# Performance work log

Measured on AMD Instinct MI355X. Metric: run time of the kernel, lower is better.

## Reference

```python
import jax, jax.numpy as jnp
import numpy as np

WIN = 5            # LNCC window_size
W_IMG = 1.0        # image_loss_weight
W_SMOOTH = 0.02    # smoothness_weight
W_JAC = 0.01       # jacobian_weight
W_INV = 0.1        # inverse_consistency_weight
EPS = 1e-05


def _avg_pool3d(x, k):
    # matches F.avg_pool3d(kernel=k, stride=1, padding=k//2, count_include_pad=True)
    p = k // 2
    s = jax.lax.reduce_window(x, jnp.array(0.0, x.dtype), jax.lax.add,
                              (1, 1, k, k, k), (1, 1, 1, 1, 1),
                              [(0, 0), (0, 0), (p, p), (p, p), (p, p)])
    return s / (k ** 3)


def _lncc(source, target):
    conv = lambda v: _avg_pool3d(v, WIN)
    sm, tm = conv(source), conv(target)
    sv = conv(source * source) - sm * sm
    tv = conv(target * target) - tm * tm
    cross = conv(source * target) - sm * tm
    lncc = cross * cross / (sv * tv + EPS)
    return jnp.nan_to_num(1.0 - lncc.mean(), nan=1.0, posinf=1.0, neginf=1.0)


def _grad3d_l2(disp):
    # Grad3D(penalty='l2'): mean squared forward differences per axis
    dz = disp[:, :, 1:] - disp[:, :, :-1]
    dy = disp[:, :, :, 1:] - disp[:, :, :, :-1]
    dx = disp[:, :, :, :, 1:] - disp[:, :, :, :, :-1]
    return (jnp.mean(dz * dz) + jnp.mean(dy * dy) + jnp.mean(dx * dx)) / 3.0


def _neg_jacobian(d):
    dx = d[:, :, 1:, :-1, :-1] - d[:, :, :-1, :-1, :-1]
    dy = d[:, :, :-1, 1:, :-1] - d[:, :, :-1, :-1, :-1]
    dz = d[:, :, :-1, :-1, 1:] - d[:, :, :-1, :-1, :-1]
    a00, a01, a02 = 1.0 + dx[:, 0], dy[:, 0], dz[:, 0]
    a10, a11, a12 = dx[:, 1], 1.0 + dy[:, 1], dz[:, 1]
    a20, a21, a22 = dx[:, 2], dy[:, 2], 1.0 + dz[:, 2]
    det = (a00 * (a11 * a22 - a12 * a21)
           - a01 * (a10 * a22 - a12 * a20)
           + a02 * (a10 * a21 - a11 * a20))
    det = jnp.nan_to_num(det, nan=0.0, posinf=1000.0, neginf=-1000.0)
    return jnp.mean(jax.nn.relu(-det))


def _warp(vol, flow):
    # SpatialTransformer: trilinear sample of vol at identity_grid + flow,
    # coordinates clamped to volume borders. vol [B,C,D,H,W], flow [B,3,D,H,W].
    B, C, D, H, W = vol.shape
    zz, yy, xx = jnp.meshgrid(jnp.arange(D, dtype=vol.dtype),
                              jnp.arange(H, dtype=vol.dtype),
                              jnp.arange(W, dtype=vol.dtype), indexing='ij')
    cz = jnp.clip(zz[None] + flow[:, 0], 0.0, D - 1)
    cy = jnp.clip(yy[None] + flow[:, 1], 0.0, H - 1)
    cx = jnp.clip(xx[None] + flow[:, 2], 0.0, W - 1)
    z0 = jnp.floor(cz); y0 = jnp.floor(cy); x0 = jnp.floor(cx)
    fz, fy, fx = cz - z0, cy - y0, cx - x0
    z0i = z0.astype(jnp.int32); y0i = y0.astype(jnp.int32); x0i = x0.astype(jnp.int32)
    z1i = jnp.minimum(z0i + 1, D - 1)
    y1i = jnp.minimum(y0i + 1, H - 1)
    x1i = jnp.minimum(x0i + 1, W - 1)
    volf = vol.reshape(B, C, D * H * W)

    def gather(zi, yi, xi):
        idx = ((zi * H + yi) * W + xi).reshape(B, 1, -1)
        idx = jnp.broadcast_to(idx, (B, C, idx.shape[-1]))
        return jnp.take_along_axis(volf, idx, axis=2).reshape(B, C, D, H, W)

    fz_, fy_, fx_ = fz[:, None], fy[:, None], fx[:, None]
    c000 = gather(z0i, y0i, x0i); c001 = gather(z0i, y0i, x1i)
    c010 = gather(z0i, y1i, x0i); c011 = gather(z0i, y1i, x1i)
    c100 = gather(z1i, y0i, x0i); c101 = gather(z1i, y0i, x1i)
    c110 = gather(z1i, y1i, x0i); c111 = gather(z1i, y1i, x1i)
    c00 = c000 * (1 - fx_) + c001 * fx_
    c01 = c010 * (1 - fx_) + c011 * fx_
    c10 = c100 * (1 - fx_) + c101 * fx_
    c11 = c110 * (1 - fx_) + c111 * fx_
    c0 = c00 * (1 - fy_) + c01 * fy_
    c1 = c10 * (1 - fy_) + c11 * fy_
    return c0 * (1 - fz_) + c1 * fz_


def _inverse_consistency(fwd, bwd):
    composed = fwd + _warp(bwd, fwd)
    return jnp.nan_to_num(jnp.mean(composed * composed), nan=0.0, posinf=1000.0, neginf=0.0)


def setup_inputs() -> dict:
    key = jax.random.key(0)
    k1, k2, k3, k4 = jax.random.split(key, 4)
    shp_img = (1, 1, 128, 128, 128)
    shp_disp = (1, 3, 128, 128, 128)
    return {
        'source': jax.random.normal(k1, shp_img, dtype=jnp.float32),
        'target': jax.random.normal(k2, shp_img, dtype=jnp.float32),
        'forward_disp': jax.random.normal(k3, shp_disp, dtype=jnp.float32),
        'backward_disp': jax.random.normal(k4, shp_disp, dtype=jnp.float32),
    }


def reference(source, target, forward_disp, backward_disp):
    total = (W_IMG * _lncc(source, target)
             + W_SMOOTH * _grad3d_l2(forward_disp)
             + W_JAC * _neg_jacobian(forward_disp)
             + W_INV * _inverse_consistency(forward_disp, backward_disp))
    return total
```

## Files before the change

### kernel.cpp

```cpp
#include <hip/hip_runtime.h>
#include <hip/hip_fp16.h>
#include <math.h>

#define DD 128
#define HH 128
#define WW 128
#define NN (DD*HH*WW)
#define DJ 127

#define NB_LNCC 4096
#define NB_FUSED 8192
#define LOFF 0
#define GOFF (NB_LNCC)
#define JOFF (NB_LNCC + NB_FUSED)
#define IOFF (NB_LNCC + 2*NB_FUSED)
#define NSLOTS (NB_LNCC + 3*NB_FUSED)
#define BWDH_OFF ((size_t)((NSLOTS * 8 + 255) & ~255))
#define WS_NEED (BWDH_OFF + (size_t)NN * 8)

struct __align__(8)  Half4 { __half x, y, z, w; };
struct __align__(16) H8  { __half2 a0, b0, a1, b1; };
struct __align__(8)  HS4 { __half2 u, v; };

__device__ __forceinline__ double wave_reduce(double v) {
    #pragma unroll
    for (int o = 32; o > 0; o >>= 1) v += __shfl_down(v, o);
    return v;
}

template <int NWAVES>
__device__ __forceinline__ double block_reduce(double v, double* red, int tid) {
    v = wave_reduce(v);
    int wid = tid >> 6, lane = tid & 63;
    __syncthreads();
    if (lane == 0) red[wid] = v;
    __syncthreads();
    double x = 0.0;
    if (tid == 0) {
        #pragma unroll
        for (int w = 0; w < NWAVES; w++) x += red[w];
    }
    return x;
}

__device__ __forceinline__ float jac_term(const float* dz_, const float* dy_, const float* dx_) {
    float a00 = 1.f + dz_[0], a01 = dy_[0], a02 = dx_[0];
    float a10 = dz_[1], a11 = 1.f + dy_[1], a12 = dx_[1];
    float a20 = dz_[2], a21 = dy_[2], a22 = 1.f + dx_[2];
    float det = a00 * (a11 * a22 - a12 * a21)
              - a01 * (a10 * a22 - a12 * a20)
              + a02 * (a10 * a21 - a11 * a20);
    if (isnan(det)) det = 0.f;
    else if (isinf(det)) det = det > 0.f ? 1000.f : -1000.f;
    float neg = -det;
    return neg > 0.f ? neg : 0.f;
}

__device__ __forceinline__ float lncc_val(float S1, float T1, float S2, float T2, float ST) {
    const float inv125 = 1.f / 125.f;
    float sm = S1 * inv125, tm = T1 * inv125;
    float sv = S2 * inv125 - sm * sm;
    float tv = T2 * inv125 - tm * tm;
    float cross = ST * inv125 - sm * tm;
    return cross * cross / (sv * tv + 1e-5f);
}

__global__ __launch_bounds__(256) void interleave4h_kernel(const float* __restrict__ bwd,
                                                           Half4* __restrict__ bwdh) {
    const int i4 = (blockIdx.x * 256 + threadIdx.x) * 4;
    float4 b0 = *(const float4*)(bwd + i4);
    float4 b1 = *(const float4*)(bwd + NN + i4);
    float4 b2 = *(const float4*)(bwd + 2 * NN + i4);
    Half4 o0 = { __float2half(b0.x), __float2half(b1.x), __float2half(b2.x), __float2half(0.f) };
    Half4 o1 = { __float2half(b0.y), __float2half(b1.y), __float2half(b2.y), __float2half(0.f) };
    Half4 o2 = { __float2half(b0.z), __float2half(b1.z), __float2half(b2.z), __float2half(0.f) };
    Half4 o3 = { __float2half(b0.w), __float2half(b1.w), __float2half(b2.w), __float2half(0.f) };
    bwdh[i4 + 0] = o0;
    bwdh[i4 + 1] = o1;
    bwdh[i4 + 2] = o2;
    bwdh[i4 + 3] = o3;
}

__global__ __launch_bounds__(256) void lncc_kernel(const float* __restrict__ src,
                                                   const float* __restrict__ tgt,
                                                   double* __restrict__ ws) {
    __shared__ H8  F1A[576];
    __shared__ HS4 F1S[288];
    __shared__ H8  F2A[384];
    __shared__ HS4 F2S[192];
    __shared__ double red[4];
    const int tid = threadIdx.x;
    const int slot = (blockIdx.x & 7) * 512 + (blockIdx.x >> 3);
    const int bz = (slot >> 8) * 8;
    const int by = ((slot >> 4) & 15) * 8;
    const int bx = (slot & 15) * 8;

    for (int t = tid; t < 288; t += 256) {
        const int h = t & 1;
        const int row = t >> 1;
        const int ly = row % 12, lz = row / 12;
        const int gy = by + ly - 2, gz = bz + lz - 2;
        const bool rowok = (gy >= 0 && gy < HH && gz >= 0 && gz < DD);
        const int rowbase = (gz * HH + gy) * WW;
        const int w0 = bx + h * 4 - 4;

        float4 lsv[3], ltv[3];
        #pragma unroll
        for (int p = 0; p < 3; p++) {
            int gx = w0 + 4 * p;
            if (rowok && gx >= 0 && gx <= WW - 4) {
                lsv[p] = *(const float4*)(src + rowbase + gx);
                ltv[p] = *(const float4*)(tgt + rowbase + gx);
            } else {
                lsv[p] = make_float4(0.f, 0.f, 0.f, 0.f);
                ltv[p] = make_float4(0.f, 0.f, 0.f, 0.f);
            }
        }
        const float* ls = (const float*)lsv;
        const float* lt = (const float*)ltv;

        float o[5][4];
        #pragma unroll
        for (int k = 0; k < 4; k++) {
            float s1 = 0.f, t1s = 0.f, s2 = 0.f, t2s = 0.f, st = 0.f;
            #pragma unroll
            for (int d = 0; d < 5; d++) {
                float a = ls[k + d + 2], b = lt[k + d + 2];
                s1 += a; t1s += b;
                s2 = fmaf(a, a, s2); t2s = fmaf(b, b, t2s); st = fmaf(a, b, st);
            }
            o[0][k] = s1; o[1][k] = t1s; o[2][k] = s2; o[3][k] = t2s; o[4][k] = st;
        }
        const int obase = (lz * 12 + ly) * 8 + h * 4;
        H8 e0 = { __floats2half2_rn(o[0][0], o[1][0]), __floats2half2_rn(o[2][0], o[3][0]),
                  __floats2half2_rn(o[0][1], o[1][1]), __floats2half2_rn(o[2][1], o[3][1]) };
        H8 e1 = { __floats2half2_rn(o[0][2], o[1][2]), __floats2half2_rn(o[2][2], o[3][2]),
                  __floats2half2_rn(o[0][3], o[1][3]), __floats2half2_rn(o[2][3], o[3][3]) };
        F1A[(obase >> 1) + 0] = e0;
        F1A[(obase >> 1) + 1] = e1;
        HS4 es = { __floats2half2_rn(o[4][0], o[4][1]), __floats2half2_rn(o[4][2], o[4][3]) };
        F1S[obase >> 2] = es;
    }
    __syncthreads();

    if (tid < 192) {
        const int h = tid & 1;
        const int r = tid >> 1;
        const int oy = r & 7, lz = r >> 3;
        const __half2 z2 = __float2half2_rn(0.f);
        __half2 A0 = z2, B0 = z2, A1 = z2, B1 = z2;
        __half2 A2 = z2, B2 = z2, A3 = z2, B3 = z2;
        __half2 S01 = z2, S23 = z2;
        #pragma unroll
        for (int dy = 0; dy < 5; dy++) {
            const int jb = (lz * 12 + oy + dy) * 8 + h * 4;
            H8 p = F1A[(jb >> 1) + 0];
            H8 q = F1A[(jb >> 1) + 1];
            A0 = __hadd2(A0, p.a0); B0 = __hadd2(B0, p.b0);
            A1 = __hadd2(A1, p.a1); B1 = __hadd2(B1, p.b1);
            A2 = __hadd2(A2, q.a0); B2 = __hadd2(B2, q.b0);
            A3 = __hadd2(A3, q.a1); B3 = __hadd2(B3, q.b1);
            HS4 s = F1S[jb >> 2];
            S01 = __hadd2(S01, s.u); S23 = __hadd2(S23, s.v);
        }
        const int jo = (lz * 8 + oy) * 8 + h * 4;
        H8 w0v = { A0, B0, A1, B1 };
        H8 w1v = { A2, B2, A3, B3 };
        F2A[(jo >> 1) + 0] = w0v;
        F2A[(jo >> 1) + 1] = w1v;
        HS4 wsv = { S01, S23 };
        F2S[jo >> 2] = wsv;
    }
    __syncthreads();

    double lsum = 0.0;
    {
        const int pos = tid * 2;
        const int oz = pos >> 6, oy = (pos >> 3) & 7, ox = pos & 7;
        const __half2 z2 = __float2half2_rn(0.f);
        __half2 cA0 = z2, cB0 = z2, cA1 = z2, cB1 = z2, cS = z2;
        #pragma unroll
        for (int dz = 0; dz < 5; dz++) {
            const int j = (((oz + dz) * 8 + oy) * 8) + ox;
            H8 p = F2A[j >> 1];
            cA0 = __hadd2(cA0, p.a0); cB0 = __hadd2(cB0, p.b0);
            cA1 = __hadd2(cA1, p.a1); cB1 = __hadd2(cB1, p.b1);
            HS4 s = F2S[j >> 2];
            cS = __hadd2(cS, (j & 2) ? s.v : s.u);
        }
        float2 s1t1_0 = __half22float2(cA0);
        float2 s2t2_0 = __half22float2(cB0);
        float2 s1t1_1 = __half22float2(cA1);
        float2 s2t2_1 = __half22float2(cB1);
        float2 stp    = __half22float2(cS);
        lsum = (double)lncc_val(s1t1_0.x, s1t1_0.y, s2t2_0.x, s2t2_0.y, stp.x)
             + (double)lncc_val(s1t1_1.x, s1t1_1.y, s2t2_1.x, s2t2_1.y, stp.y);
    }
    double tot = block_reduce<4>(lsum, red, tid);
    if (tid == 0) ws[LOFF + slot] = tot;
}

__global__ __launch_bounds__(256, 4) void fused1h_kernel(const float* __restrict__ fwd,
                                                         const Half4* __restrict__ bwdh,
                                                         double* __restrict__ ws) {
    __shared__ double red[4];

    const int swz = (blockIdx.x & 7) * (NB_FUSED / 8) + (blockIdx.x >> 3);
    const int idx = swz * 256 + threadIdx.x;
    const int x = idx & 127; const int y = (idx >> 7) & 127; const int z = idx >> 14;
    const bool hx = (x < WW - 1), hy = (y < HH - 1), hz = (z < DD - 1);

    double accG = 0.0, accJ = 0.0, accI = 0.0;

    float v[3], ddx[3], ddy[3], ddz[3];
    #pragma unroll
    for (int c = 0; c < 3; c++) {
        const float* p = fwd + c * NN + idx;
        float vv = p[0];
        v[c]   = vv;
        ddx[c] = hx ? (p[1] - vv) : 0.f;
        ddy[c] = hy ? (p[WW] - vv) : 0.f;
        ddz[c] = hz ? (p[HH * WW] - vv) : 0.f;
    }

    {
        float g = 0.f;
        #pragma unroll
        for (int c = 0; c < 3; c++)
            g = fmaf(ddz[c], ddz[c], fmaf(ddy[c], ddy[c], fmaf(ddx[c], ddx[c], g)));
        accG = (double)g;
    }

    if (hx && hy && hz) accJ = (double)jac_term(ddz, ddy, ddx);

    {
        float cz = fminf(fmaxf((float)z + v[0], 0.f), (float)(DD - 1));
        float cy = fminf(fmaxf((float)y + v[1], 0.f), (float)(HH - 1));
        float cx = fminf(fmaxf((float)x + v[2], 0.f), (float)(WW - 1));
        float z0f = floorf(cz), y0f = floorf(cy), x0f = floorf(cx);
        float fz = cz - z0f, fy = cy - y0f, fx = cx - x0f;
        int z0 = (int)z0f, y0 = (int)y0f, x0 = (int)x0f;
        int z1 = min(z0 + 1, DD - 1), y1 = min(y0 + 1, HH - 1), x1 = min(x0 + 1, WW - 1);
        int b00 = (z0 * HH + y0) * WW, b01 = (z0 * HH + y1) * WW;
        int b10 = (z1 * HH + y0) * WW, b11 = (z1 * HH + y1) * WW;
        Half4 H000 = bwdh[b00 + x0], H001 = bwdh[b00 + x1];
        Half4 H010 = bwdh[b01 + x0], H011 = bwdh[b01 + x1];
        Half4 H100 = bwdh[b10 + x0], H101 = bwdh[b10 + x1];
        Half4 H110 = bwdh[b11 + x0], H111 = bwdh[b11 + x1];
        float w000 = (1.f - fz) * (1.f - fy) * (1.f - fx);
        float w001 = (1.f - fz) * (1.f - fy) * fx;
        float w010 = (1.f - fz) * fy * (1.f - fx);
        float w011 = (1.f - fz) * fy * fx;
        float w100 = fz * (1.f - fy) * (1.f - fx);
        float w101 = fz * (1.f - fy) * fx;
        float w110 = fz * fy * (1.f - fx);
        float w111 = fz * fy * fx;
        float c0 = v[0] + w000 * __half2float(H000.x) + w001 * __half2float(H001.x)
                        + w010 * __half2float(H010.x) + w011 * __half2float(H011.x)
                        + w100 * __half2float(H100.x) + w101 * __half2float(H101.x)
                        + w110 * __half2float(H110.x) + w111 * __half2float(H111.x);
        float c1 = v[1] + w000 * __half2float(H000.y) + w001 * __half2float(H001.y)
                        + w010 * __half2float(H010.y) + w011 * __half2float(H011.y)
                        + w100 * __half2float(H100.y) + w101 * __half2float(H101.y)
                        + w110 * __half2float(H110.y) + w111 * __half2float(H111.y);
        float c2 = v[2] + w000 * __half2float(H000.z) + w001 * __half2float(H001.z)
                        + w010 * __half2float(H010.z) + w011 * __half2float(H011.z)
                        + w100 * __half2float(H100.z) + w101 * __half2float(H101.z)
                        + w110 * __half2float(H110.z) + w111 * __half2float(H111.z);
        accI = (double)(c0 * c0 + c1 * c1 + c2 * c2);
    }

    double tG = block_reduce<4>(accG, red, threadIdx.x);
    double tJ = block_reduce<4>(accJ, red, threadIdx.x);
    double tI = block_reduce<4>(accI, red, threadIdx.x);
    if (threadIdx.x == 0) {
        ws[GOFF + swz] = tG;
        ws[JOFF + swz] = tJ;
        ws[IOFF + swz] = tI;
    }
}

__global__ __launch_bounds__(256) void fused_fallback(const float* __restrict__ fwd,
                                                      const float* __restrict__ bwd,
                                                      double* __restrict__ ws) {
    __shared__ double red[4];
    const int idx = blockIdx.x * 256 + threadIdx.x;
    const int x = idx & 127; const int y = (idx >> 7) & 127; const int z = idx >> 14;
    const bool hx = (x < WW - 1), hy = (y < HH - 1), hz = (z < DD - 1);

    double accG = 0.0, accJ = 0.0, accI = 0.0;
    float v[3], ddx[3], ddy[3], ddz[3];
    #pragma unroll
    for (int c = 0; c < 3; c++) {
        const float* p = fwd + c * NN + idx;
        float vv = p[0];
        v[c]   = vv;
        ddx[c] = hx ? (p[1] - vv) : 0.f;
        ddy[c] = hy ? (p[WW] - vv) : 0.f;
        ddz[c] = hz ? (p[HH * WW] - vv) : 0.f;
    }
    float g = 0.f;
    #pragma unroll
    for (int c = 0; c < 3; c++)
        g = fmaf(ddz[c], ddz[c], fmaf(ddy[c], ddy[c], fmaf(ddx[c], ddx[c], g)));
    accG = (double)g;
    if (hx && hy && hz) accJ = (double)jac_term(ddz, ddy, ddx);
    {
        float cz = fminf(fmaxf((float)z + v[0], 0.f), (float)(DD - 1));
        float cy = fminf(fmaxf((float)y + v[1], 0.f), (float)(HH - 1));
        float cx = fminf(fmaxf((float)x + v[2], 0.f), (float)(WW - 1));
        float z0f = floorf(cz), y0f = floorf(cy), x0f = floorf(cx);
        float fz = cz - z0f, fy = cy - y0f, fx = cx - x0f;
        int z0 = (int)z0f, y0 = (int)y0f, x0 = (int)x0f;
        int z1 = min(z0 + 1, DD - 1), y1 = min(y0 + 1, HH - 1), x1 = min(x0 + 1, WW - 1);
        int i000 = (z0 * HH + y0) * WW + x0, i001 = (z0 * HH + y0) * WW + x1;
        int i010 = (z0 * HH + y1) * WW + x0, i011 = (z0 * HH + y1) * WW + x1;
        int i100 = (z1 * HH + y0) * WW + x0, i101 = (z1 * HH + y0) * WW + x1;
        int i110 = (z1 * HH + y1) * WW + x0, i111 = (z1 * HH + y1) * WW + x1;
        float w000 = (1.f - fz) * (1.f - fy) * (1.f - fx);
        float w001 = (1.f - fz) * (1.f - fy) * fx;
        float w010 = (1.f - fz) * fy * (1.f - fx);
        float w011 = (1.f - fz) * fy * fx;
        float w100 = fz * (1.f - fy) * (1.f - fx);
        float w101 = fz * (1.f - fy) * fx;
        float w110 = fz * fy * (1.f - fx);
        float w111 = fz * fy * fx;
        #pragma unroll
        for (int c = 0; c < 3; c++) {
            const float* b = bwd + c * NN;
            float warped = w000 * b[i000] + w001 * b[i001]
                         + w010 * b[i010] + w011 * b[i011]
                         + w100 * b[i100] + w101 * b[i101]
                         + w110 * b[i110] + w111 * b[i111];
            float comp = v[c] + warped;
            accI += (double)(comp * comp);
        }
    }

    double tG = block_reduce<4>(accG, red, threadIdx.x);
    double tJ = block_reduce<4>(accJ, red, threadIdx.x);
    double tI = block_reduce<4>(accI, red, threadIdx.x);
    if (threadIdx.x == 0) {
        ws[GOFF + blockIdx.x] = tG;
        ws[JOFF + blockIdx.x] = tJ;
        ws[IOFF + blockIdx.x] = tI;
    }
}

__global__ __launch_bounds__(256) void finalize_kernel(const double* __restrict__ ws,
                                                       float* __restrict__ out) {
    __shared__ double red[4];
    double l = 0.0, g = 0.0, j = 0.0, inv = 0.0;
    for (int k = threadIdx.x; k < NB_LNCC; k += 256) l += ws[LOFF + k];
    for (int k = threadIdx.x; k < NB_FUSED; k += 256) {
        g   += ws[GOFF + k];
        j   += ws[JOFF + k];
        inv += ws[IOFF + k];
    }
    double tl = block_reduce<4>(l, red, threadIdx.x);
    double tg = block_reduce<4>(g, red, threadIdx.x);
    double tj = block_reduce<4>(j, red, threadIdx.x);
    double ti = block_reduce<4>(inv, red, threadIdx.x);
    if (threadIdx.x == 0) {
        double li = 1.0 - tl / (double)NN;
        if (isnan(li) || isinf(li)) li = 1.0;
        double grad = tg / (9.0 * 127.0 * 128.0 * 128.0);
        double jac  = tj / ((double)DJ * DJ * DJ);
        double iv = ti / (3.0 * (double)NN);
        if (isnan(iv)) iv = 0.0;
        else if (isinf(iv)) iv = iv > 0.0 ? 1000.0 : 0.0;
        out[0] = (float)(1.0 * li + 0.02 * grad + 0.01 * jac + 0.1 * iv);
    }
}

extern "C" void kernel_launch(void* const* d_in, const int* in_sizes, int n_in,
                              void* d_out, int out_size, void* d_ws, size_t ws_size,
                              hipStream_t stream) {
    const float* src = (const float*)d_in[0];
    const float* tgt = (const float*)d_in[1];
    const float* fwd = (const float*)d_in[2];
    const float* bwd = (const float*)d_in[3];
    double* ws = (double*)d_ws;
    float* out = (float*)d_out;

    if (ws_size >= WS_NEED) {
        Half4* bwdh = (Half4*)((char*)d_ws + BWDH_OFF);
        interleave4h_kernel<<<2048, 256, 0, stream>>>(bwd, bwdh);
        lncc_kernel<<<4096, 256, 0, stream>>>(src, tgt, ws);
        fused1h_kernel<<<NB_FUSED, 256, 0, stream>>>(fwd, bwdh, ws);
    } else {
        lncc_kernel<<<4096, 256, 0, stream>>>(src, tgt, ws);
        fused_fallback<<<NB_FUSED, 256, 0, stream>>>(fwd, bwd, ws);
    }
    finalize_kernel<<<1, 256, 0, stream>>>(ws, out);
}
```

Measured before the change: 83.35 us.

## Store x-neighbor pairs of half backward field to halve warp gathers

After: 90.48 us. 1.09x slower.

```diff
diff --git a/kernel.cpp b/kernel.cpp
--- a/kernel.cpp
+++ b/kernel.cpp
@@ -15,10 +15,10 @@
 #define JOFF (NB_LNCC + NB_FUSED)
 #define IOFF (NB_LNCC + 2*NB_FUSED)
 #define NSLOTS (NB_LNCC + 3*NB_FUSED)
-#define BWDH_OFF ((size_t)((NSLOTS * 8 + 255) & ~255))
-#define WS_NEED (BWDH_OFF + (size_t)NN * 8)
-
-struct __align__(8)  Half4 { __half x, y, z, w; };
+#define BWDP_OFF ((size_t)((NSLOTS * 8 + 255) & ~255))
+#define ENT_O (NN/2)
+#define WS_NEED (BWDP_OFF + (size_t)NN * 16)
+
 struct __align__(16) H8  { __half2 a0, b0, a1, b1; };
 struct __align__(8)  HS4 { __half2 u, v; };
 
@@ -65,20 +65,42 @@
     return cross * cross / (sv * tv + 1e-5f);
 }
 
-__global__ __launch_bounds__(256) void interleave4h_kernel(const float* __restrict__ bwd,
-                                                           Half4* __restrict__ bwdh) {
-    const int i4 = (blockIdx.x * 256 + threadIdx.x) * 4;
+__device__ __forceinline__ float4 pack2(float a0, float a1, float a2,
+                                        float c0, float c1, float c2) {
+    union { float4 f; __half2 h[4]; } u;
+    u.h[0] = __floats2half2_rn(a0, a1);
+    u.h[1] = __floats2half2_rn(a2, 0.f);
+    u.h[2] = __floats2half2_rn(c0, c1);
+    u.h[3] = __floats2half2_rn(c2, 0.f);
+    return u.f;
+}
+
+__device__ __forceinline__ void unpack_mix(float4 L, float fx,
+                                           float& o0, float& o1, float& o2) {
+    union { float4 f; __half2 h[4]; } u; u.f = L;
+    float2 p01 = __half22float2(u.h[0]);
+    float2 p2_ = __half22float2(u.h[1]);
+    float2 q01 = __half22float2(u.h[2]);
+    float2 q2_ = __half22float2(u.h[3]);
+    o0 = fmaf(fx, q01.x - p01.x, p01.x);
+    o1 = fmaf(fx, q01.y - p01.y, p01.y);
+    o2 = fmaf(fx, q2_.x - p2_.x, p2_.x);
+}
+
+__global__ __launch_bounds__(256) void interleave_pair_kernel(const float* __restrict__ bwd,
+                                                              float4* __restrict__ bwdp) {
+    const int t = blockIdx.x * 256 + threadIdx.x;
+    const int i4 = t * 4;
     float4 b0 = *(const float4*)(bwd + i4);
     float4 b1 = *(const float4*)(bwd + NN + i4);
     float4 b2 = *(const float4*)(bwd + 2 * NN + i4);
-    Half4 o0 = { __float2half(b0.x), __float2half(b1.x), __float2half(b2.x), __float2half(0.f) };
-    Half4 o1 = { __float2half(b0.y), __float2half(b1.y), __float2half(b2.y), __float2half(0.f) };
-    Half4 o2 = { __float2half(b0.z), __float2half(b1.z), __float2half(b2.z), __float2half(0.f) };
-    Half4 o3 = { __float2half(b0.w), __float2half(b1.w), __float2half(b2.w), __float2half(0.f) };
-    bwdh[i4 + 0] = o0;
-    bwdh[i4 + 1] = o1;
-    bwdh[i4 + 2] = o2;
-    bwdh[i4 + 3] = o3;
+    const int inext = (i4 + 4 < NN) ? i4 + 4 : NN - 1;
+    float n0 = bwd[inext], n1 = bwd[NN + inext], n2 = bwd[2 * NN + inext];
+
+    bwdp[2 * t + 0]         = pack2(b0.x, b1.x, b2.x, b0.y, b1.y, b2.y);
+    bwdp[2 * t + 1]         = pack2(b0.z, b1.z, b2.z, b0.w, b1.w, b2.w);
+    bwdp[ENT_O + 2 * t + 0] = pack2(b0.y, b1.y, b2.y, b0.z, b1.z, b2.z);
+    bwdp[ENT_O + 2 * t + 1] = pack2(b0.w, b1.w, b2.w, n0, n1, n2);
 }
 
 __global__ __launch_bounds__(256) void lncc_kernel(const float* __restrict__ src,
@@ -200,17 +222,17 @@
     if (tid == 0) ws[LOFF + slot] = tot;
 }
 
-__global__ __launch_bounds__(256, 4) void fused1h_kernel(const float* __restrict__ fwd,
-                                                         const Half4* __restrict__ bwdh,
+__global__ __launch_bounds__(256, 4) void fused1p_kernel(const float* __restrict__ fwd,
+                                                         const float4* __restrict__ bwdp,
                                                          double* __restrict__ ws) {
-    __shared__ double red[4];
+    __shared__ double red[12];
 
     const int swz = (blockIdx.x & 7) * (NB_FUSED / 8) + (blockIdx.x >> 3);
     const int idx = swz * 256 + threadIdx.x;
     const int x = idx & 127; const int y = (idx >> 7) & 127; const int z = idx >> 14;
     const bool hx = (x < WW - 1), hy = (y < HH - 1), hz = (z < DD - 1);
 
-    double accG = 0.0, accJ = 0.0, accI = 0.0;
+    double accG, accJ, accI = 0.0;
 
     float v[3], ddx[3], ddy[3], ddz[3];
     #pragma unroll
@@ -231,7 +253,7 @@
         accG = (double)g;
     }
 
-    if (hx && hy && hz) accJ = (double)jac_term(ddz, ddy, ddx);
+    accJ = (hx && hy && hz) ? (double)jac_term(ddz, ddy, ddx) : 0.0;
 
     {
         float cz = fminf(fmaxf((float)z + v[0], 0.f), (float)(DD - 1));
@@ -240,43 +262,42 @@
         float z0f = floorf(cz), y0f = floorf(cy), x0f = floorf(cx);
         float fz = cz - z0f, fy = cy - y0f, fx = cx - x0f;
         int z0 = (int)z0f, y0 = (int)y0f, x0 = (int)x0f;
-        int z1 = min(z0 + 1, DD - 1), y1 = min(y0 + 1, HH - 1), x1 = min(x0 + 1, WW - 1);
-        int b00 = (z0 * HH + y0) * WW, b01 = (z0 * HH + y1) * WW;
-        int b10 = (z1 * HH + y0) * WW, b11 = (z1 * HH + y1) * WW;
-        Half4 H000 = bwdh[b00 + x0], H001 = bwdh[b00 + x1];
-        Half4 H010 = bwdh[b01 + x0], H011 = bwdh[b01 + x1];
-        Half4 H100 = bwdh[b10 + x0], H101 = bwdh[b10 + x1];
-        Half4 H110 = bwdh[b11 + x0], H111 = bwdh[b11 + x1];
-        float w000 = (1.f - fz) * (1.f - fy) * (1.f - fx);
-        float w001 = (1.f - fz) * (1.f - fy) * fx;
-        float w010 = (1.f - fz) * fy * (1.f - fx);
-        float w011 = (1.f - fz) * fy * fx;
-        float w100 = fz * (1.f - fy) * (1.f - fx);
-        float w101 = fz * (1.f - fy) * fx;
-        float w110 = fz * fy * (1.f - fx);
-        float w111 = fz * fy * fx;
-        float c0 = v[0] + w000 * __half2float(H000.x) + w001 * __half2float(H001.x)
-                        + w010 * __half2float(H010.x) + w011 * __half2float(H011.x)
-                        + w100 * __half2float(H100.x) + w101 * __half2float(H101.x)
-                        + w110 * __half2float(H110.x) + w111 * __half2float(H111.x);
-        float c1 = v[1] + w000 * __half2float(H000.y) + w001 * __half2float(H001.y)
-                        + w010 * __half2float(H010.y) + w011 * __half2float(H011.y)
-                        + w100 * __half2float(H100.y) + w101 * __half2float(H101.y)
-                        + w110 * __half2float(H110.y) + w111 * __half2float(H111.y);
-        float c2 = v[2] + w000 * __half2float(H000.z) + w001 * __half2float(H001.z)
-                        + w010 * __half2float(H010.z) + w011 * __half2float(H011.z)
-                        + w100 * __half2float(H100.z) + w101 * __half2float(H101.z)
-                        + w110 * __half2float(H110.z) + w111 * __half2float(H111.z);
+        int z1 = min(z0 + 1, DD - 1), y1 = min(y0 + 1, HH - 1);
+
+        const int xe = x0 >> 1;
+        const int po = (x0 & 1) ? ENT_O : 0;
+        const int r00 = (z0 * HH + y0) * 64, r01 = (z0 * HH + y1) * 64;
+        const int r10 = (z1 * HH + y0) * 64, r11 = (z1 * HH + y1) * 64;
+        float4 L00 = bwdp[po + r00 + xe];
+        float4 L01 = bwdp[po + r01 + xe];
+        float4 L10 = bwdp[po + r10 + xe];
+        float4 L11 = bwdp[po + r11 + xe];
+
+        float m00_0, m00_1, m00_2, m01_0, m01_1, m01_2;
+        float m10_0, m10_1, m10_2, m11_0, m11_1, m11_2;
+        unpack_mix(L00, fx, m00_0, m00_1, m00_2);
+        unpack_mix(L01, fx, m01_0, m01_1, m01_2);
+        unpack_mix(L10, fx, m10_0, m10_1, m10_2);
+        unpack_mix(L11, fx, m11_0, m11_1, m11_2);
+
+        float w00 = (1.f - fz) * (1.f - fy), w01 = (1.f - fz) * fy;
+        float w10 = fz * (1.f - fy),         w11 = fz * fy;
+        float c0 = v[0] + w00 * m00_0 + w01 * m01_0 + w10 * m10_0 + w11 * m11_0;
+        float c1 = v[1] + w00 * m00_1 + w01 * m01_1 + w10 * m10_1 + w11 * m11_1;
+        float c2 = v[2] + w00 * m00_2 + w01 * m01_2 + w10 * m10_2 + w11 * m11_2;
         accI = (double)(c0 * c0 + c1 * c1 + c2 * c2);
     }
 
-    double tG = block_reduce<4>(accG, red, threadIdx.x);
-    double tJ = block_reduce<4>(accJ, red, threadIdx.x);
-    double tI = block_reduce<4>(accI, red, threadIdx.x);
+    accG = wave_reduce(accG);
+    accJ = wave_reduce(accJ);
+    accI = wave_reduce(accI);
+    const int wid = threadIdx.x >> 6, lane = threadIdx.x & 63;
+    if (lane == 0) { red[wid] = accG; red[4 + wid] = accJ; red[8 + wid] = accI; }
+    __syncthreads();
     if (threadIdx.x == 0) {
-        ws[GOFF + swz] = tG;
-        ws[JOFF + swz] = tJ;
-        ws[IOFF + swz] = tI;
+        ws[GOFF + swz] = red[0] + red[1] + red[2] + red[3];
+        ws[JOFF + swz] = red[4] + red[5] + red[6] + red[7];
+        ws[IOFF + swz] = red[8] + red[9] + red[10] + red[11];
     }
 }
 
@@ -384,10 +405,10 @@
     float* out = (float*)d_out;
 
     if (ws_size >= WS_NEED) {
-        Half4* bwdh = (Half4*)((char*)d_ws + BWDH_OFF);
-        interleave4h_kernel<<<2048, 256, 0, stream>>>(bwd, bwdh);
+        float4* bwdp = (float4*)((char*)d_ws + BWDP_OFF);
+        interleave_pair_kernel<<<2048, 256, 0, stream>>>(bwd, bwdp);
         lncc_kernel<<<4096, 256, 0, stream>>>(src, tgt, ws);
-        fused1h_kernel<<<NB_FUSED, 256, 0, stream>>>(fwd, bwdh, ws);
+        fused1p_kernel<<<NB_FUSED, 256, 0, stream>>>(fwd, bwdp, ws);
     } else {
         lncc_kernel<<<4096, 256, 0, stream>>>(src, tgt, ws);
         fused_fallback<<<NB_FUSED, 256, 0, stream>>>(fwd, bwd, ws);
```
